# Kernel tuning notes

Measured on AMD Instinct MI355X. Metric: run time of the kernel, lower is better.

Reference implementation:

```python
import jax, jax.numpy as jnp
import numpy as np

B, S, DM, H, DF = 2, 2048, 1024, 16, 4096
HD = DM // H
EPS = 1e-6
NEG = -1e9


def setup_inputs() -> dict:
    key = jax.random.key(0)
    ks = jax.random.split(key, 16)
    sc = 1.0 / np.sqrt(DM)
    scf = 1.0 / np.sqrt(DF)
    return {
        "x": jax.random.normal(ks[0], (B, S, DM), jnp.float32),
        "src_mask": jax.random.randint(ks[1], (B, 1, 1, S), 0, 2, jnp.int32),
        "Wq": jax.random.normal(ks[2], (DM, DM), jnp.float32) * sc,
        "bq": jnp.zeros((DM,), jnp.float32),
        "Wk": jax.random.normal(ks[3], (DM, DM), jnp.float32) * sc,
        "bk": jnp.zeros((DM,), jnp.float32),
        "Wv": jax.random.normal(ks[4], (DM, DM), jnp.float32) * sc,
        "bv": jnp.zeros((DM,), jnp.float32),
        "Wo": jax.random.normal(ks[5], (DM, DM), jnp.float32) * sc,
        "bo": jnp.zeros((DM,), jnp.float32),
        "W1": jax.random.normal(ks[6], (DM, DF), jnp.float32) * sc,
        "b1": jnp.zeros((DF,), jnp.float32),
        "W2": jax.random.normal(ks[7], (DF, DM), jnp.float32) * scf,
        "b2": jnp.zeros((DM,), jnp.float32),
        "alpha1": jnp.ones((1,), jnp.float32),
        "beta1": jnp.ones((1,), jnp.float32),
        "alpha2": jnp.ones((1,), jnp.float32),
        "beta2": jnp.ones((1,), jnp.float32),
    }


def layer_norm(x, alpha, beta):
    # torch: mean + unbiased std (ddof=1), scalar alpha/beta, eps added to std
    mean = jnp.mean(x, axis=-1, keepdims=True)
    std = jnp.std(x, axis=-1, keepdims=True, ddof=1)
    return alpha * (x - mean) / (std + EPS) + beta


def mha(x, mask, Wq, bq, Wk, bk, Wv, bv, Wo, bo):
    def split(t):  # [B,S,DM] -> [B,H,S,HD]
        return t.reshape(B, S, H, HD).transpose(0, 2, 1, 3)
    q = split(x @ Wq + bq)
    k = split(x @ Wk + bk)
    v = split(x @ Wv + bv)
    scores = jnp.einsum("bhqd,bhkd->bhqk", q, k) / np.sqrt(HD)
    scores = jnp.where(mask == 0, NEG, scores)
    probs = jax.nn.softmax(scores, axis=-1)  # dropout in eval mode = identity
    out = jnp.einsum("bhqk,bhkd->bhqd", probs, v)
    out = out.transpose(0, 2, 1, 3).reshape(B, S, DM)
    return out @ Wo + bo


def reference(x, src_mask, Wq, bq, Wk, bk, Wv, bv, Wo, bo, W1, b1, W2, b2,
              alpha1, beta1, alpha2, beta2):
    # pre-norm residual: x + attn(norm(x)); dropout disabled (eval)
    n1 = layer_norm(x, alpha1, beta1)
    h = x + mha(n1, src_mask, Wq, bq, Wk, bk, Wv, bv, Wo, bo)
    n2 = layer_norm(h, alpha2, beta2)
    ff = jax.nn.relu(n2 @ W1 + b1) @ W2 + b2
    return h + ff
```

## Files before the change

### kernel.cpp

```cpp
#include <hip/hip_runtime.h>
#include <hip/hip_bf16.h>

#define SEQ   2048
#define BATCH 2
#define DMODEL 1024
#define DFF   4096
#define NHEAD 16
#define HDIM  64
#define NTOK  (BATCH*SEQ)

typedef short s8v __attribute__((ext_vector_type(8)));
typedef float f4v __attribute__((ext_vector_type(4)));

__device__ __forceinline__ float b2f(unsigned short u) {
    union { unsigned int i; float f; } v; v.i = ((unsigned int)u) << 16; return v.f;
}
__device__ __forceinline__ unsigned short f2b(float f) {
    union { unsigned int i; float f; } v; v.f = f;
    unsigned int r = v.i + 0x7FFFu + ((v.i >> 16) & 1u);
    return (unsigned short)(r >> 16);
}
__device__ __forceinline__ ushort2 cvt_pk(float a, float b) {
    __hip_bfloat162 h = __float22bfloat162_rn(float2{ a, b });
    return *(ushort2*)&h;
}

__device__ __forceinline__ f4v mfma_bf16(s8v a, s8v b, f4v c) {
    return __builtin_amdgcn_mfma_f32_16x16x32_bf16(a, b, c, 0, 0, 0);
}

__device__ __forceinline__ void gload_lds16(const void* g, void* l) {
    __builtin_amdgcn_global_load_lds(
        (const __attribute__((address_space(1))) unsigned int*)g,
        (__attribute__((address_space(3))) unsigned int*)l, 16, 0, 0);
}

template<int N> __device__ __forceinline__ void wait_vmcnt() {
    if constexpr (N == 8)      asm volatile("s_waitcnt vmcnt(8)" ::: "memory");
    else if constexpr (N == 6) asm volatile("s_waitcnt vmcnt(6)" ::: "memory");
    else if constexpr (N == 4) asm volatile("s_waitcnt vmcnt(4)" ::: "memory");
    else if constexpr (N == 2) asm volatile("s_waitcnt vmcnt(2)" ::: "memory");
    else                       asm volatile("s_waitcnt vmcnt(0)" ::: "memory");
}

__device__ __forceinline__ void tp_tile(const float* __restrict__ src,
                                        unsigned short* __restrict__ dst,
                                        int R, int C, int br, int bc, int t,
                                        unsigned short* tl) {
    for (int i = 0; i < 4; i++) {
        int lin = i * 1024 + t * 4;
        int r = lin >> 6, c = lin & 63;
        float4 u = *(const float4*)&src[(size_t)(br * 64 + r) * C + bc * 64 + c];
        tl[r * 65 + c + 0] = f2b(u.x);
        tl[r * 65 + c + 1] = f2b(u.y);
        tl[r * 65 + c + 2] = f2b(u.z);
        tl[r * 65 + c + 3] = f2b(u.w);
    }
    __syncthreads();
    for (int i = 0; i < 4; i++) {
        int lin = i * 1024 + t * 4;
        int r2 = lin >> 6, c2 = lin & 63;
        ushort4 o;
        o.x = tl[(c2 + 0) * 65 + r2];
        o.y = tl[(c2 + 1) * 65 + r2];
        o.z = tl[(c2 + 2) * 65 + r2];
        o.w = tl[(c2 + 3) * 65 + r2];
        *(ushort4*)&dst[(size_t)(bc * 64 + r2) * R + br * 64 + c2] = o;
    }
}

__global__ __launch_bounds__(256) void prep_weights(const float* __restrict__ Wq,
                                                    const float* __restrict__ Wk,
                                                    const float* __restrict__ Wv,
                                                    const float* __restrict__ Wo,
                                                    const float* __restrict__ W1,
                                                    const float* __restrict__ W2,
                                                    const float* __restrict__ bq,
                                                    const float* __restrict__ bk,
                                                    const float* __restrict__ bv,
                                                    const float* __restrict__ x,
                                                    const float* __restrict__ a1,
                                                    const float* __restrict__ be1,
                                                    unsigned short* __restrict__ Wqkv_t,
                                                    unsigned short* __restrict__ Wo_t,
                                                    unsigned short* __restrict__ W1_t,
                                                    unsigned short* __restrict__ W2_t,
                                                    float* __restrict__ bqkv,
                                                    unsigned short* __restrict__ n1) {
    __shared__ unsigned short tl[64 * 65];
    __shared__ float red[8];
    const int t = threadIdx.x;
    const int bx = blockIdx.x, by = blockIdx.y, z = blockIdx.z;
    if (z < 4) {
        const float* src = (z == 0) ? Wq : (z == 1) ? Wk : (z == 2) ? Wv : Wo;
        unsigned short* dst = (z == 3) ? Wo_t : Wqkv_t + (size_t)z * 1024 * 1024;
        tp_tile(src, dst, 1024, 1024, bx, by, t, tl);
    } else if (z == 4) {
        for (int i = 0; i < 4; i++) {
            tp_tile(W1, W1_t, 1024, 4096, bx, by + 16 * i, t, tl);
            __syncthreads();
        }
    } else if (z == 5) {
        if (bx == 0 && by == 0) {
            for (int i = 0; i < 12; i++) {
                int idx = t + 256 * i;
                if (idx < 1024) bqkv[idx] = bq[idx];
                else if (idx < 2048) bqkv[idx] = bk[idx - 1024];
                else if (idx < 3072) bqkv[idx] = bv[idx - 2048];
            }
        }
        for (int i = 0; i < 4; i++) {
            tp_tile(W2, W2_t, 4096, 1024, bx + 16 * i, by, t, tl);
            __syncthreads();
        }
    } else {
        const int row = (z - 6) * 256 + by * 16 + bx;
        const float* xr = x + (size_t)row * DMODEL;
        float4 u = ((const float4*)xr)[t];
        float v[4] = { u.x, u.y, u.z, u.w };
        float s = v[0] + v[1] + v[2] + v[3];
        float sq = v[0]*v[0] + v[1]*v[1] + v[2]*v[2] + v[3]*v[3];
        for (int off = 32; off; off >>= 1) { s += __shfl_xor(s, off); sq += __shfl_xor(sq, off); }
        int wave = t >> 6, lane = t & 63;
        if (!lane) { red[wave] = s; red[4 + wave] = sq; }
        __syncthreads();
        s = red[0] + red[1] + red[2] + red[3];
        sq = red[4] + red[5] + red[6] + red[7];
        float mean = s * (1.f / DMODEL);
        float var = (sq - (float)DMODEL * mean * mean) * (1.f / (DMODEL - 1));
        var = var < 0.f ? 0.f : var;
        float inv = a1[0] / (sqrtf(var) + 1e-6f);
        float bt = be1[0];
        uint2 ou;
        unsigned short r0 = f2b((v[0] - mean) * inv + bt);
        unsigned short r1 = f2b((v[1] - mean) * inv + bt);
        unsigned short r2 = f2b((v[2] - mean) * inv + bt);
        unsigned short r3 = f2b((v[3] - mean) * inv + bt);
        ou.x = (unsigned int)r0 | ((unsigned int)r1 << 16);
        ou.y = (unsigned int)r2 | ((unsigned int)r3 << 16);
        ((uint2*)(n1 + (size_t)row * DMODEL))[t] = ou;
    }
}

__global__ __launch_bounds__(256) void mask_scan(const int* __restrict__ msk,
                                                 int* __restrict__ idx,
                                                 float* __restrict__ maskc2,
                                                 int* __restrict__ ntiles) {
    const int b = blockIdx.x, t = threadIdx.x;
    const int base = b * SEQ;
    __shared__ int wsum[4];
    int k[8]; int cnt = 0;
    for (int j = 0; j < 8; j++) {
        k[j] = (msk[base + t * 8 + j] != 0) ? 1 : 0;
        cnt += k[j];
    }
    const int lane = t & 63, wv = t >> 6;
    int pre = cnt;
    for (int off = 1; off < 64; off <<= 1) {
        int n = __shfl_up(pre, off);
        if (lane >= off) pre += n;
    }
    if (lane == 63) wsum[wv] = pre;
    __syncthreads();
    const int Nb = wsum[0] + wsum[1] + wsum[2] + wsum[3];
    int woff = 0;
    for (int w = 0; w < wv; w++) woff += wsum[w];
    const int excl = woff + pre - cnt;
    for (int j = 0; j < 8; j++) {
        int g = t * 8 + j;
        idx[base + g] = 0;
        maskc2[base + g] = (g < Nb) ? 0.f : -1e9f;
    }
    __syncthreads();
    int pos = excl;
    for (int j = 0; j < 8; j++) {
        if (k[j]) { idx[base + pos] = t * 8 + j; pos++; }
    }
    if (t == 0) ntiles[b] = (Nb + 63) >> 6;
}

__global__ __launch_bounds__(256) void pack_kv(const unsigned short* __restrict__ Kb,
                                               const unsigned short* __restrict__ Vb,
                                               const int* __restrict__ idx,
                                               const int* __restrict__ ntiles,
                                               unsigned short* __restrict__ Kc,
                                               unsigned short* __restrict__ Vc) {
    __shared__ unsigned short tl[64 * 65];
    const int t = threadIdx.x;
    const int kt = blockIdx.x, h = blockIdx.y, b = blockIdx.z;
    if (kt >= ntiles[b]) return;
    const int* idxb = idx + b * SEQ + kt * 64;
    const unsigned short* srcK = Kb + (size_t)b * SEQ * 1024 + h * HDIM;
    unsigned short* dstK = Kc + ((size_t)((b * NHEAD + h) * 32 + kt)) * 4096;
    for (int i = 0; i < 2; i++) {
        int ci = t + 256 * i;
        int r = ci >> 3, cp = ci & 7;
        int cl = cp ^ (r & 7);
        int row = idxb[r];
        *(uint4*)&dstK[ci * 8] = *(const uint4*)&srcK[(size_t)row * 1024 + cl * 8];
    }
    const unsigned short* srcV = Vb + (size_t)b * SEQ * 1024 + h * HDIM;
    for (int i = 0; i < 16; i++) {
        int idx2 = t + 256 * i;
        int r = idx2 >> 6, c = idx2 & 63;
        int row = idxb[r];
        tl[r * 65 + c] = srcV[(size_t)row * 1024 + c];
    }
    __syncthreads();
    unsigned short* dstV = Vc + ((size_t)((b * NHEAD + h) * 32 + kt)) * 4096;
    for (int i = 0; i < 2; i++) {
        int ci = t + 256 * i;
        int r = ci >> 3, cp = ci & 7;
        int cl = cp ^ (r & 7);
        ushort4 e0, e1;
        e0.x = tl[(cl * 8 + 0) * 65 + r]; e0.y = tl[(cl * 8 + 1) * 65 + r];
        e0.z = tl[(cl * 8 + 2) * 65 + r]; e0.w = tl[(cl * 8 + 3) * 65 + r];
        e1.x = tl[(cl * 8 + 4) * 65 + r]; e1.y = tl[(cl * 8 + 5) * 65 + r];
        e1.z = tl[(cl * 8 + 6) * 65 + r]; e1.w = tl[(cl * 8 + 7) * 65 + r];
        *(ushort4*)&dstV[ci * 8]     = e0;
        *(ushort4*)&dstV[ci * 8 + 4] = e1;
    }
}

__global__ __launch_bounds__(256) void ln_add(float* __restrict__ hb,
                                              const float* __restrict__ pbuf,
                                              const float* __restrict__ al,
                                              const float* __restrict__ be,
                                              unsigned short* __restrict__ o) {
    const int row = blockIdx.x;
    float* hr = hb + (size_t)row * DMODEL;
    const float* pr = pbuf + (size_t)row * DMODEL;
    float4 u = ((const float4*)hr)[threadIdx.x];
    float4 p = ((const float4*)pr)[threadIdx.x];
    u.x += p.x; u.y += p.y; u.z += p.z; u.w += p.w;
    ((float4*)hr)[threadIdx.x] = u;
    float v[4] = { u.x, u.y, u.z, u.w };
    float s = v[0] + v[1] + v[2] + v[3];
    float sq = v[0]*v[0] + v[1]*v[1] + v[2]*v[2] + v[3]*v[3];
    for (int off = 32; off; off >>= 1) { s += __shfl_xor(s, off); sq += __shfl_xor(sq, off); }
    __shared__ float red[8];
    int wave = threadIdx.x >> 6, lane = threadIdx.x & 63;
    if (!lane) { red[wave] = s; red[4 + wave] = sq; }
    __syncthreads();
    s = red[0] + red[1] + red[2] + red[3];
    sq = red[4] + red[5] + red[6] + red[7];
    float mean = s * (1.f / DMODEL);
    float var = (sq - (float)DMODEL * mean * mean) * (1.f / (DMODEL - 1));
    var = var < 0.f ? 0.f : var;
    float inv = al[0] / (sqrtf(var) + 1e-6f);
    float bt = be[0];
    uint2 ou;
    unsigned short r0 = f2b((v[0] - mean) * inv + bt);
    unsigned short r1 = f2b((v[1] - mean) * inv + bt);
    unsigned short r2 = f2b((v[2] - mean) * inv + bt);
    unsigned short r3 = f2b((v[3] - mean) * inv + bt);
    ou.x = (unsigned int)r0 | ((unsigned int)r1 << 16);
    ou.y = (unsigned int)r2 | ((unsigned int)r3 << 16);
    ((uint2*)(o + (size_t)row * DMODEL))[threadIdx.x] = ou;
}

__global__ __launch_bounds__(256) void add_pbuf(float* __restrict__ out,
                                                const float* __restrict__ pbuf) {
    const int i0 = (blockIdx.x * 256 + threadIdx.x) * 8;
    float4 a0 = *(const float4*)&out[i0];
    float4 a1 = *(const float4*)&out[i0 + 4];
    float4 p0 = *(const float4*)&pbuf[i0];
    float4 p1 = *(const float4*)&pbuf[i0 + 4];
    a0.x += p0.x; a0.y += p0.y; a0.z += p0.z; a0.w += p0.w;
    a1.x += p1.x; a1.y += p1.y; a1.z += p1.z; a1.w += p1.w;
    *(float4*)&out[i0]     = a0;
    *(float4*)&out[i0 + 4] = a1;
}

template<int SPAN, int NL>
__device__ __forceinline__ void stage_half(const unsigned short* __restrict__ mat,
                                           int base, int K, int k0, int q,
                                           unsigned short* sdst, int t) {
#pragma unroll
    for (int i = 0; i < NL; i++) {
        int ci = i * 512 + t;
        int rl = ci >> 3;
        int c  = (ci & 7) ^ (rl & 7);
        int gr = (rl / SPAN) * (2 * SPAN) + q * SPAN + (rl % SPAN);
        gload_lds16(mat + (size_t)(base + gr) * K + k0 + c * 8, sdst + (size_t)ci * 8);
    }
}

__device__ __forceinline__ const s8v* afrag(const unsigned short* sA, int mi, int s,
                                            int wm, int l16, int quad) {
    int q = mi >> 2;
    int rl = wm * 64 + (mi & 3) * 16 + l16;
    return (const s8v*)&sA[q * 8192 + rl * 64 + (((s * 4 + quad) ^ (l16 & 7)) * 8)];
}
__device__ __forceinline__ const s8v* bfrag(const unsigned short* sB, int ni, int s,
                                            int wn, int l16, int quad) {
    int q = ni >> 1;
    int rl = wn * 32 + (ni & 1) * 16 + l16;
    return (const s8v*)&sB[q * 8192 + rl * 64 + (((s * 4 + quad) ^ (l16 & 7)) * 8)];
}

__device__ __forceinline__ void half_8ph(const unsigned short* __restrict__ A,
                                         const unsigned short* __restrict__ Bt,
                                         int m0, int n0, int K, int kT1, int kT2, bool doT2,
                                         const unsigned short* sAr, const unsigned short* sBr,
                                         unsigned short* sA_this, unsigned short* sB_this,
                                         unsigned short* sA_oth,
                                         int wm, int wn, int l16, int quad, int t,
                                         f4v acc[8][4]) {
    s8v a[4][2], b[4][2];
#pragma unroll
    for (int m2 = 0; m2 < 4; m2++) {
        a[m2][0] = *afrag(sAr, m2, 0, wm, l16, quad);
        a[m2][1] = *afrag(sAr, m2, 1, wm, l16, quad);
    }
#pragma unroll
    for (int nb = 0; nb < 2; nb++) {
        b[nb][0] = *bfrag(sBr, nb, 0, wn, l16, quad);
        b[nb][1] = *bfrag(sBr, nb, 1, wn, l16, quad);
    }
    stage_half<64, 2>(A, m0, K, kT1, 1, sA_oth + 8192, t);
    __builtin_amdgcn_s_barrier();
    asm volatile("s_waitcnt lgkmcnt(0)" ::: "memory");
    __builtin_amdgcn_s_setprio(1);
#pragma unroll
    for (int m2 = 0; m2 < 4; m2++)
#pragma unroll
        for (int nb = 0; nb < 2; nb++) {
            acc[m2][nb] = mfma_bf16(a[m2][0], b[nb][0], acc[m2][nb]);
            acc[m2][nb] = mfma_bf16(a[m2][1], b[nb][1], acc[m2][nb]);
        }
    __builtin_amdgcn_s_setprio(0);
    __builtin_amdgcn_s_barrier();
#pragma unroll
    for (int nb = 0; nb < 2; nb++) {
        b[2 + nb][0] = *bfrag(sBr, 2 + nb, 0, wn, l16, quad);
        b[2 + nb][1] = *bfrag(sBr, 2 + nb, 1, wn, l16, quad);
    }
    if (doT2) stage_half<64, 2>(A, m0, K, kT2, 0, sA_this, t);
    __builtin_amdgcn_s_barrier();
    asm volatile("s_waitcnt lgkmcnt(0)" ::: "memory");
    __builtin_amdgcn_s_setprio(1);
#pragma unroll
    for (int m2 = 0; m2 < 4; m2++)
#pragma unroll
        for (int nb = 0; nb < 2; nb++) {
            acc[m2][2 + nb] = mfma_bf16(a[m2][0], b[2 + nb][0], acc[m2][2 + nb]);
            acc[m2][2 + nb] = mfma_bf16(a[m2][1], b[2 + nb][1], acc[m2][2 + nb]);
        }
    __builtin_amdgcn_s_setprio(0);
    __builtin_amdgcn_s_barrier();
#pragma unroll
    for (int m2 = 0; m2 < 4; m2++) {
        a[m2][0] = *afrag(sAr, 4 + m2, 0, wm, l16, quad);
        a[m2][1] = *afrag(sAr, 4 + m2, 1, wm, l16, quad);
    }
    if (doT2) stage_half<32, 2>(Bt, n0, K, kT2, 0, sB_this, t);
    __builtin_amdgcn_s_barrier();
    asm volatile("s_waitcnt lgkmcnt(0)" ::: "memory");
    __builtin_amdgcn_s_setprio(1);
#pragma unroll
    for (int m2 = 0; m2 < 4; m2++)
#pragma unroll
        for (int nb = 0; nb < 2; nb++) {
            acc[4 + m2][nb] = mfma_bf16(a[m2][0], b[nb][0], acc[4 + m2][nb]);
            acc[4 + m2][nb] = mfma_bf16(a[m2][1], b[nb][1], acc[4 + m2][nb]);
        }
    __builtin_amdgcn_s_setprio(0);
    __builtin_amdgcn_s_barrier();
    if (doT2) {
        stage_half<32, 2>(Bt, n0, K, kT2, 1, sB_this + 8192, t);
        wait_vmcnt<6>();
    } else {
        wait_vmcnt<0>();
    }
    __builtin_amdgcn_s_barrier();
    __builtin_amdgcn_s_setprio(1);
#pragma unroll
    for (int m2 = 0; m2 < 4; m2++)
#pragma unroll
        for (int nb = 0; nb < 2; nb++) {
            acc[4 + m2][2 + nb] = mfma_bf16(a[m2][0], b[2 + nb][0], acc[4 + m2][2 + nb]);
            acc[4 + m2][2 + nb] = mfma_bf16(a[m2][1], b[2 + nb][1], acc[4 + m2][2 + nb]);
        }
    __builtin_amdgcn_s_setprio(0);
    __builtin_amdgcn_s_barrier();
}

__device__ __forceinline__ void comp_full(const unsigned short* sA, const unsigned short* sB,
                                          int wm, int wn, int l16, int quad,
                                          f4v acc[8][4]) {
    s8v b[4][2];
#pragma unroll
    for (int ni = 0; ni < 4; ni++) {
        b[ni][0] = *bfrag(sB, ni, 0, wn, l16, quad);
        b[ni][1] = *bfrag(sB, ni, 1, wn, l16, quad);
    }
#pragma unroll
    for (int mi = 0; mi < 8; mi++) {
        s8v a0 = *afrag(sA, mi, 0, wm, l16, quad);
        s8v a1 = *afrag(sA, mi, 1, wm, l16, quad);
#pragma unroll
        for (int ni = 0; ni < 4; ni++) {
            acc[mi][ni] = mfma_bf16(a0, b[ni][0], acc[mi][ni]);
            acc[mi][ni] = mfma_bf16(a1, b[ni][1], acc[mi][ni]);
        }
    }
}

template<bool RELU, typename CT, bool SPLIT3>
__global__ __launch_bounds__(512, 2) void gemm256(const unsigned short* __restrict__ A,
                                                  const unsigned short* __restrict__ Bt,
                                                  const float* __restrict__ bias,
                                                  CT* __restrict__ C,
                                                  int M, int N, int K) {
    __shared__ __align__(16) unsigned short smA[2][256 * 64];
    __shared__ __align__(16) unsigned short smB[2][256 * 64];
    const int t = threadIdx.x;
    const int wave = t >> 6, lane = t & 63;
    const int quad = lane >> 4, l16 = lane & 15;
    const int wm = wave >> 2, wn = wave & 3;
    const int m0 = blockIdx.x * 256, n0 = blockIdx.y * 256;
    const int nt = K >> 6;

    f4v acc[8][4] = {};

    stage_half<64, 2>(A, m0, K, 0, 0, smA[0], t);
    stage_half<64, 2>(A, m0, K, 0, 1, smA[0] + 8192, t);
    stage_half<32, 2>(Bt, n0, K, 0, 0, smB[0], t);
    stage_half<32, 2>(Bt, n0, K, 0, 1, smB[0] + 8192, t);
    stage_half<64, 2>(A, m0, K, 64, 0, smA[1], t);
    stage_half<32, 2>(Bt, n0, K, 64, 0, smB[1], t);
    stage_half<32, 2>(Bt, n0, K, 64, 1, smB[1] + 8192, t);
    wait_vmcnt<6>();
    __builtin_amdgcn_s_barrier();

    for (int i = 0; i < nt / 2 - 1; ++i) {
        const int kb = 2 * i * 64;
        half_8ph(A, Bt, m0, n0, K, kb + 64, kb + 128, true,
                 smA[0], smB[0], smA[0], smB[0], smA[1],
                 wm, wn, l16, quad, t, acc);
        half_8ph(A, Bt, m0, n0, K, kb + 128, kb + 192, true,
                 smA[1], smB[1], smA[1], smB[1], smA[0],
                 wm, wn, l16, quad, t, acc);
    }
    half_8ph(A, Bt, m0, n0, K, (nt - 1) * 64, 0, false,
             smA[0], smB[0], smA[0], smB[0], smA[1],
             wm, wn, l16, quad, t, acc);
    __builtin_amdgcn_s_setprio(1);
    comp_full(smA[1], smB[1], wm, wn, l16, quad, acc);
    __builtin_amdgcn_s_setprio(0);

#pragma unroll
    for (int mi = 0; mi < 8; mi++) {
#pragma unroll
        for (int ni = 0; ni < 4; ni++) {
            const int col = n0 + wn * 64 + ni * 16 + l16;
            const int row0 = m0 + wm * 128 + mi * 16 + quad * 4;
            const float bv = bias[col];
#pragma unroll
            for (int r = 0; r < 4; r++) {
                float v = acc[mi][ni][r] + bv;
                if (RELU) v = v > 0.f ? v : 0.f;
                size_t cidx;
                if constexpr (SPLIT3)
                    cidx = (size_t)(col >> 10) * ((size_t)NTOK * 1024)
                         + (size_t)row0 * 1024 + (size_t)r * 1024 + (col & 1023);
                else
                    cidx = (size_t)(row0 + r) * N + col;
                if constexpr (sizeof(CT) == 2)
                    C[cidx] = f2b(v);
                else
                    C[cidx] = v;
            }
        }
    }
}


__device__ __forceinline__ void stage128(const unsigned short* __restrict__ mat,
                                         int base, int K, int k0,
                                         unsigned short* sdst, int t) {
#pragma unroll
    for (int q = 0; q < 2; q++) {
        int rl = t >> 3;
        int c  = (t & 7) ^ (rl & 7);
        gload_lds16(mat + (size_t)(base + q * 64 + rl) * K + k0 + c * 8,
                    sdst + q * 4096 + (size_t)t * 8);
    }
}

__device__ __forceinline__ s8v rdfrag128(const unsigned short* sm, int q, int fi,
                                         int l16, int quad, int sW) {
    int rl = fi * 16 + l16;
    int p = (sW * 4 + quad) ^ (l16 & 7);
    return *(const s8v*)&sm[q * 4096 + rl * 64 + p * 8];
}

__global__ __launch_bounds__(512, 4) void gemm128k(const unsigned short* __restrict__ A,
                                                   const unsigned short* __restrict__ Bt,
                                                   const float* __restrict__ bias,
                                                   const float* __restrict__ res,
                                                   float* __restrict__ C,
                                                   float* __restrict__ pbuf,
                                                   int M, int N, int K, int KS) {
    __shared__ __align__(16) unsigned short smem[4][8192];
    const int t = threadIdx.x;
    const int wave = t >> 6, lane = t & 63;
    const int quad = lane >> 4, l16 = lane & 15;
    const int sW = wave >> 2, wm = (wave >> 1) & 1, wn = wave & 1;
    const int m0 = blockIdx.x * 128, n0 = blockIdx.y * 128;
    const int z = blockIdx.z;
    const int kbeg = z * KS;
    const int nt = KS >> 6;

    f4v acc[4][4] = {};

    stage128(A,  m0, K, kbeg,      smem[0], t);
    stage128(Bt, n0, K, kbeg,      smem[2], t);
    stage128(A,  m0, K, kbeg + 64, smem[1], t);
    stage128(Bt, n0, K, kbeg + 64, smem[3], t);
    wait_vmcnt<4>();
    __builtin_amdgcn_s_barrier();

    for (int it = 0; it < nt; ++it) {
        const int cb = it & 1;
        const unsigned short* sA = smem[cb];
        const unsigned short* sB = smem[2 + cb];
        s8v a[4], b[4];
#pragma unroll
        for (int i = 0; i < 4; i++) a[i] = rdfrag128(sA, wm, i, l16, quad, sW);
#pragma unroll
        for (int i = 0; i < 4; i++) b[i] = rdfrag128(sB, wn, i, l16, quad, sW);
        asm volatile("s_waitcnt lgkmcnt(0)" ::: "memory");
        __builtin_amdgcn_s_setprio(1);
#pragma unroll
        for (int mi = 0; mi < 4; mi++)
#pragma unroll
            for (int ni = 0; ni < 4; ni++)
                acc[mi][ni] = mfma_bf16(a[mi], b[ni], acc[mi][ni]);
        __builtin_amdgcn_s_setprio(0);
        __builtin_amdgcn_s_barrier();
        if (it + 2 < nt) {
            stage128(A,  m0, K, kbeg + (it + 2) * 64, smem[cb], t);
            stage128(Bt, n0, K, kbeg + (it + 2) * 64, smem[2 + cb], t);
            wait_vmcnt<4>();
        } else if (it + 1 < nt) {
            wait_vmcnt<0>();
        }
        __builtin_amdgcn_s_barrier();
    }

    float* xch = (float*)&smem[0][0];
    float* myx = xch + (wm * 2 + wn) * 4096;
    if (sW == 1) {
#pragma unroll
        for (int mi = 0; mi < 4; mi++)
#pragma unroll
            for (int ni = 0; ni < 4; ni++)
                *(f4v*)&myx[(mi * 4 + ni) * 256 + lane * 4] = acc[mi][ni];
    }
    __builtin_amdgcn_s_barrier();
    if (sW == 0) {
#pragma unroll
        for (int mi = 0; mi < 4; mi++)
#pragma unroll
            for (int ni = 0; ni < 4; ni++)
                acc[mi][ni] += *(const f4v*)&myx[(mi * 4 + ni) * 256 + lane * 4];
#pragma unroll
        for (int mi = 0; mi < 4; mi++)
#pragma unroll
            for (int ni = 0; ni < 4; ni++) {
                const int col = n0 + wn * 64 + ni * 16 + l16;
                const int row0 = m0 + wm * 64 + mi * 16 + quad * 4;
                if (z == 0) {
                    const float bv = bias[col];
#pragma unroll
                    for (int r = 0; r < 4; r++) {
                        size_t ix = (size_t)(row0 + r) * N + col;
                        C[ix] = acc[mi][ni][r] + bv + res[ix];
                    }
                } else {
#pragma unroll
                    for (int r = 0; r < 4; r++)
                        pbuf[(size_t)(row0 + r) * N + col] = acc[mi][ni][r];
                }
            }
    }
}

#define EXPC 0.18033688f
__device__ __forceinline__ void attn_tile(const unsigned short* __restrict__ smKb,
                                          const unsigned short* __restrict__ smVb,
                                          const float* __restrict__ smM, int k0,
                                          unsigned short* __restrict__ smPw,
                                          s8v qf0, s8v qf1, int quad, int l16,
                                          float& l_s, f4v* oacc) {
    const int l7 = l16 & 7;
    f4v s[4];
#pragma unroll
    for (int kt4 = 0; kt4 < 4; kt4++) {
        int r = kt4 * 16 + l16;
        s8v kf0 = *(const s8v*)&smKb[r * 64 + ((quad ^ l7) * 8)];
        s8v kf1 = *(const s8v*)&smKb[r * 64 + (((quad + 4) ^ l7) * 8)];
        f4v z = {};
        z = mfma_bf16(kf0, qf0, z);
        z = mfma_bf16(kf1, qf1, z);
        s[kt4] = z;
    }
#pragma unroll
    for (int kt4 = 0; kt4 < 4; kt4++) {
        float4 mf = *(const float4*)&smM[k0 + kt4 * 16 + quad * 4];
        s[kt4][0] = s[kt4][0] * EXPC + mf.x;
        s[kt4][1] = s[kt4][1] * EXPC + mf.y;
        s[kt4][2] = s[kt4][2] * EXPC + mf.z;
        s[kt4][3] = s[kt4][3] * EXPC + mf.w;
    }
#pragma unroll
    for (int kt4 = 0; kt4 < 4; kt4++)
#pragma unroll
        for (int r = 0; r < 4; r++) {
            float p = __builtin_amdgcn_exp2f(s[kt4][r]);
            s[kt4][r] = p;
            l_s += p;
        }
#pragma unroll
    for (int kt4 = 0; kt4 < 4; kt4++) {
        ushort2 p01 = cvt_pk(s[kt4][0], s[kt4][1]);
        ushort2 p23 = cvt_pk(s[kt4][2], s[kt4][3]);
        ushort4 pk;
        pk.x = p01.x; pk.y = p01.y; pk.z = p23.x; pk.w = p23.y;
        int c = kt4 * 2 + (quad >> 1);
        *(ushort4*)&smPw[l16 * 64 + ((c ^ l7) * 8 + (quad & 1) * 4)] = pk;
    }
    s8v pf0 = *(const s8v*)&smPw[l16 * 64 + ((quad ^ l7) * 8)];
    s8v pf1 = *(const s8v*)&smPw[l16 * 64 + (((quad + 4) ^ l7) * 8)];
#pragma unroll
    for (int nt = 0; nt < 4; nt++) {
        int r = nt * 16 + l16;
        s8v v0 = *(const s8v*)&smVb[r * 64 + ((quad ^ l7) * 8)];
        s8v v1 = *(const s8v*)&smVb[r * 64 + (((quad + 4) ^ l7) * 8)];
        oacc[nt] = mfma_bf16(pf0, v0, oacc[nt]);
        oacc[nt] = mfma_bf16(pf1, v1, oacc[nt]);
    }
}

__global__ __launch_bounds__(512) void attn_kernel(const unsigned short* __restrict__ Qb,
                                                   const unsigned short* __restrict__ Kc,
                                                   const unsigned short* __restrict__ Vc,
                                                   const float* __restrict__ maskc2,
                                                   const int* __restrict__ ntiles,
                                                   unsigned short* __restrict__ out) {
    __shared__ __align__(16) unsigned short smK[2][4096];
    __shared__ __align__(16) unsigned short smV[2][4096];
    __shared__ __align__(16) unsigned short smP[8][1024];
    __shared__ __align__(16) float smM[SEQ];

    const int t = threadIdx.x;
    const int wave = t >> 6, lane = t & 63;
    const int quad = lane >> 4, l16 = lane & 15;
    const int qt = blockIdx.x, h = blockIdx.y, b = blockIdx.z;
    const int q0 = qt * 128 + wave * 16;
    const int nt = ntiles[b];
    const unsigned short* Kbh = Kc + ((size_t)(b * NHEAD + h)) * 32 * 4096;
    const unsigned short* Vbh = Vc + ((size_t)(b * NHEAD + h)) * 32 * 4096;
    unsigned short* smPw = &smP[wave][0];

    const unsigned short* Qp = Qb + ((size_t)b * SEQ + q0 + l16) * 1024 + h * HDIM + quad * 8;
    s8v qf0 = *(const s8v*)(Qp);
    s8v qf1 = *(const s8v*)(Qp + 32);

    gload_lds16(maskc2 + (size_t)b * SEQ + t * 4, (float*)smM + t * 4);
    gload_lds16(Kbh + t * 8,        smK[0] + t * 8);
    gload_lds16(Vbh + t * 8,        smV[0] + t * 8);
    gload_lds16(Kbh + 4096 + t * 8, smK[1] + t * 8);
    gload_lds16(Vbh + 4096 + t * 8, smV[1] + t * 8);
    wait_vmcnt<2>();
    __builtin_amdgcn_s_barrier();

    float l_s = 0.f;
    f4v oacc[4] = {};

    for (int it = 0; it < nt; ++it) {
        const int cb = it & 1;
        __builtin_amdgcn_s_setprio(1);
        attn_tile(smK[cb], smV[cb], smM, it * 64, smPw, qf0, qf1, quad, l16, l_s, oacc);
        __builtin_amdgcn_s_setprio(0);
        if (it + 2 < nt) {
            asm volatile("s_waitcnt lgkmcnt(0)" ::: "memory");
            __builtin_amdgcn_s_barrier();
            gload_lds16(Kbh + (size_t)(it + 2) * 4096 + t * 8, smK[cb] + t * 8);
            gload_lds16(Vbh + (size_t)(it + 2) * 4096 + t * 8, smV[cb] + t * 8);
            wait_vmcnt<2>();
            __builtin_amdgcn_s_barrier();
        } else if (it + 1 < nt) {
            asm volatile("s_waitcnt lgkmcnt(0)" ::: "memory");
            __builtin_amdgcn_s_barrier();
            wait_vmcnt<0>();
            __builtin_amdgcn_s_barrier();
        }
    }

    l_s += __shfl_xor(l_s, 16);
    l_s += __shfl_xor(l_s, 32);
    float lrr[4];
    for (int r = 0; r < 4; r++) lrr[r] = __shfl(l_s, quad * 4 + r);
    for (int nt2 = 0; nt2 < 4; nt2++)
        for (int r = 0; r < 4; r++) {
            int row = q0 + quad * 4 + r;
            int col = h * HDIM + nt2 * 16 + l16;
            out[((size_t)b * SEQ + row) * DMODEL + col] = f2b(oacc[nt2][r] / lrr[r]);
        }
}

extern "C" void kernel_launch(void* const* d_in, const int* in_sizes, int n_in,
                              void* d_out, int out_size, void* d_ws, size_t ws_size,
                              hipStream_t stream) {
    const float* x   = (const float*)d_in[0];
    const int*   msk = (const int*)d_in[1];
    const float* Wq  = (const float*)d_in[2];
    const float* bq  = (const float*)d_in[3];
    const float* Wk  = (const float*)d_in[4];
    const float* bk  = (const float*)d_in[5];
    const float* Wv  = (const float*)d_in[6];
    const float* bv  = (const float*)d_in[7];
    const float* Wo  = (const float*)d_in[8];
    const float* bo  = (const float*)d_in[9];
    const float* W1  = (const float*)d_in[10];
    const float* b1  = (const float*)d_in[11];
    const float* W2  = (const float*)d_in[12];
    const float* b2  = (const float*)d_in[13];
    const float* a1  = (const float*)d_in[14];
    const float* be1 = (const float*)d_in[15];
    const float* a2  = (const float*)d_in[16];
    const float* be2 = (const float*)d_in[17];
    float* outf = (float*)d_out;

    char* ws = (char*)d_ws;
    const size_t MB = 1024 * 1024;
    unsigned short* W2_t   = (unsigned short*)(ws);
    unsigned short* W1_t   = (unsigned short*)(ws + 8 * MB);
    float*          Pbuf   = (float*)(ws + 8 * MB);
    unsigned short* Wqkv_t = (unsigned short*)(ws + 16 * MB);
    float*          bqkv   = (float*)(ws + 22 * MB);
    unsigned short* Kc     = (unsigned short*)(ws + 16 * MB);
    unsigned short* n2     = (unsigned short*)(ws + 16 * MB);
    unsigned short* Wo_t   = (unsigned short*)(ws + 24 * MB);
    unsigned short* Qb     = (unsigned short*)(ws + 26 * MB);
    unsigned short* Kb     = (unsigned short*)(ws + 34 * MB);
    unsigned short* Vb     = (unsigned short*)(ws + 42 * MB);
    float*          Pbuf2  = (float*)(ws + 34 * MB);
    unsigned short* ff1    = (unsigned short*)(ws + 26 * MB);
    unsigned short* attnO  = (unsigned short*)(ws + 50 * MB);
    unsigned short* n1     = (unsigned short*)d_out;
    unsigned short* Vc     = (unsigned short*)d_out;
    float*          hbuf   = (float*)d_out;
    float*          maskc2 = (float*)((char*)d_out + 8 * MB);
    int*            idxc   = (int*)((char*)d_out + 8 * MB + 16 * 1024);
    int*            ntl    = (int*)((char*)d_out + 8 * MB + 32 * 1024);

    mask_scan<<<dim3(BATCH), 256, 0, stream>>>(msk, idxc, maskc2, ntl);
    prep_weights<<<dim3(16, 16, 22), 256, 0, stream>>>(
        Wq, Wk, Wv, Wo, W1, W2, bq, bk, bv, x, a1, be1,
        Wqkv_t, Wo_t, W1_t, W2_t, bqkv, n1);

    gemm256<false, unsigned short, true><<<dim3(16, 12), 512, 0, stream>>>(
        n1, Wqkv_t, bqkv, Qb, NTOK, 3072, 1024);
    pack_kv<<<dim3(32, 16, 2), 256, 0, stream>>>(Kb, Vb, idxc, ntl, Kc, Vc);
    attn_kernel<<<dim3(16, 16, 2), 512, 0, stream>>>(Qb, Kc, Vc, maskc2, ntl, attnO);
    gemm128k<<<dim3(32, 8, 2), 512, 0, stream>>>(
        attnO, Wo_t, bo, x, hbuf, Pbuf2, NTOK, 1024, 1024, 512);
    ln_add<<<NTOK, 256, 0, stream>>>(hbuf, Pbuf2, a2, be2, n2);
    gemm256<true, unsigned short, false><<<dim3(16, 16), 512, 0, stream>>>(
        n2, W1_t, b1, ff1, NTOK, DFF, 1024);
    gemm128k<<<dim3(32, 8, 2), 512, 0, stream>>>(
        ff1, W2_t, b2, hbuf, outf, Pbuf, NTOK, 1024, 4096, 2048);
    add_pbuf<<<dim3(2048), 256, 0, stream>>>(outf, Pbuf);
}
```

Before: 327.5 us.

## Fold mask scan into prep kernel, swizzle block order, move LDS wait after MFMAs

```diff
diff --git a/kernel.cpp b/kernel.cpp
--- a/kernel.cpp
+++ b/kernel.cpp
@@ -81,14 +81,19 @@
                                                     const float* __restrict__ x,
                                                     const float* __restrict__ a1,
                                                     const float* __restrict__ be1,
+                                                    const int* __restrict__ msk,
                                                     unsigned short* __restrict__ Wqkv_t,
                                                     unsigned short* __restrict__ Wo_t,
                                                     unsigned short* __restrict__ W1_t,
                                                     unsigned short* __restrict__ W2_t,
                                                     float* __restrict__ bqkv,
-                                                    unsigned short* __restrict__ n1) {
+                                                    unsigned short* __restrict__ n1,
+                                                    int* __restrict__ idxc,
+                                                    float* __restrict__ maskc2,
+                                                    int* __restrict__ ntl) {
     __shared__ unsigned short tl[64 * 65];
     __shared__ float red[8];
+    __shared__ int wsum[4];
     const int t = threadIdx.x;
     const int bx = blockIdx.x, by = blockIdx.y, z = blockIdx.z;
     if (z < 4) {
@@ -113,6 +118,38 @@
             tp_tile(W2, W2_t, 4096, 1024, bx + 16 * i, by, t, tl);
             __syncthreads();
         }
+    } else if (z == 22) {
+        if (bx >= BATCH || by != 0) return;
+        const int b = bx;
+        const int base = b * SEQ;
+        int k[8]; int cnt = 0;
+        for (int j = 0; j < 8; j++) {
+            k[j] = (msk[base + t * 8 + j] != 0) ? 1 : 0;
+            cnt += k[j];
+        }
+        const int lane = t & 63, wv = t >> 6;
+        int pre = cnt;
+        for (int off = 1; off < 64; off <<= 1) {
+            int n = __shfl_up(pre, off);
+            if (lane >= off) pre += n;
+        }
+        if (lane == 63) wsum[wv] = pre;
+        __syncthreads();
+        const int Nb = wsum[0] + wsum[1] + wsum[2] + wsum[3];
+        int woff = 0;
+        for (int w = 0; w < wv; w++) woff += wsum[w];
+        const int excl = woff + pre - cnt;
+        for (int j = 0; j < 8; j++) {
+            int g = t * 8 + j;
+            idxc[base + g] = 0;
+            maskc2[base + g] = (g < Nb) ? 0.f : -1e9f;
+        }
+        __syncthreads();
+        int pos = excl;
+        for (int j = 0; j < 8; j++) {
+            if (k[j]) { idxc[base + pos] = t * 8 + j; pos++; }
+        }
+        if (t == 0) ntl[b] = (Nb + 63) >> 6;
     } else {
         const int row = (z - 6) * 256 + by * 16 + bx;
         const float* xr = x + (size_t)row * DMODEL;
@@ -140,43 +177,6 @@
         ou.y = (unsigned int)r2 | ((unsigned int)r3 << 16);
         ((uint2*)(n1 + (size_t)row * DMODEL))[t] = ou;
     }
-}
-
-__global__ __launch_bounds__(256) void mask_scan(const int* __restrict__ msk,
-                                                 int* __restrict__ idx,
-                                                 float* __restrict__ maskc2,
-                                                 int* __restrict__ ntiles) {
-    const int b = blockIdx.x, t = threadIdx.x;
-    const int base = b * SEQ;
-    __shared__ int wsum[4];
-    int k[8]; int cnt = 0;
-    for (int j = 0; j < 8; j++) {
-        k[j] = (msk[base + t * 8 + j] != 0) ? 1 : 0;
-        cnt += k[j];
-    }
-    const int lane = t & 63, wv = t >> 6;
-    int pre = cnt;
-    for (int off = 1; off < 64; off <<= 1) {
-        int n = __shfl_up(pre, off);
-        if (lane >= off) pre += n;
-    }
-    if (lane == 63) wsum[wv] = pre;
-    __syncthreads();
-    const int Nb = wsum[0] + wsum[1] + wsum[2] + wsum[3];
-    int woff = 0;
-    for (int w = 0; w < wv; w++) woff += wsum[w];
-    const int excl = woff + pre - cnt;
-    for (int j = 0; j < 8; j++) {
-        int g = t * 8 + j;
-        idx[base + g] = 0;
-        maskc2[base + g] = (g < Nb) ? 0.f : -1e9f;
-    }
-    __syncthreads();
-    int pos = excl;
-    for (int j = 0; j < 8; j++) {
-        if (k[j]) { idx[base + pos] = t * 8 + j; pos++; }
-    }
-    if (t == 0) ntiles[b] = (Nb + 63) >> 6;
 }
 
 __global__ __launch_bounds__(256) void pack_kv(const unsigned short* __restrict__ Kb,
@@ -464,7 +464,7 @@
                 size_t cidx;
                 if constexpr (SPLIT3)
                     cidx = (size_t)(col >> 10) * ((size_t)NTOK * 1024)
-                         + (size_t)row0 * 1024 + (size_t)r * 1024 + (col & 1023);
+                         + (size_t)(row0 + r) * 1024 + (col & 1023);
                 else
                     cidx = (size_t)(row0 + r) * N + col;
                 if constexpr (sizeof(CT) == 2)
@@ -508,8 +508,11 @@
     const int wave = t >> 6, lane = t & 63;
     const int quad = lane >> 4, l16 = lane & 15;
     const int sW = wave >> 2, wm = (wave >> 1) & 1, wn = wave & 1;
-    const int m0 = blockIdx.x * 128, n0 = blockIdx.y * 128;
-    const int z = blockIdx.z;
+    const int lin = blockIdx.x + (blockIdx.y << 6);
+    const int swz = (lin & 7) * 64 + (lin >> 3);
+    const int z  = swz & 1;
+    const int m0 = ((swz >> 1) & 31) * 128;
+    const int n0 = (swz >> 6) * 128;
     const int kbeg = z * KS;
     const int nt = KS >> 6;
 
@@ -531,7 +534,6 @@
         for (int i = 0; i < 4; i++) a[i] = rdfrag128(sA, wm, i, l16, quad, sW);
 #pragma unroll
         for (int i = 0; i < 4; i++) b[i] = rdfrag128(sB, wn, i, l16, quad, sW);
-        asm volatile("s_waitcnt lgkmcnt(0)" ::: "memory");
         __builtin_amdgcn_s_setprio(1);
 #pragma unroll
         for (int mi = 0; mi < 4; mi++)
@@ -539,6 +541,7 @@
             for (int ni = 0; ni < 4; ni++)
                 acc[mi][ni] = mfma_bf16(a[mi], b[ni], acc[mi][ni]);
         __builtin_amdgcn_s_setprio(0);
+        asm volatile("s_waitcnt lgkmcnt(0)" ::: "memory");
         __builtin_amdgcn_s_barrier();
         if (it + 2 < nt) {
             stage128(A,  m0, K, kbeg + (it + 2) * 64, smem[cb], t);
@@ -658,7 +661,9 @@
     const int t = threadIdx.x;
     const int wave = t >> 6, lane = t & 63;
     const int quad = lane >> 4, l16 = lane & 15;
-    const int qt = blockIdx.x, h = blockIdx.y, b = blockIdx.z;
+    const int lin = blockIdx.x + (blockIdx.y << 4) + (blockIdx.z << 8);
+    const int swz = (lin & 7) * 64 + (lin >> 3);
+    const int qt = swz & 15, h = (swz >> 4) & 15, b = swz >> 8;
     const int q0 = qt * 128 + wave * 16;
     const int nt = ntiles[b];
     const unsigned short* Kbh = Kc + ((size_t)(b * NHEAD + h)) * 32 * 4096;
@@ -758,21 +763,20 @@
     int*            idxc   = (int*)((char*)d_out + 8 * MB + 16 * 1024);
     int*            ntl    = (int*)((char*)d_out + 8 * MB + 32 * 1024);
 
-    mask_scan<<<dim3(BATCH), 256, 0, stream>>>(msk, idxc, maskc2, ntl);
-    prep_weights<<<dim3(16, 16, 22), 256, 0, stream>>>(
-        Wq, Wk, Wv, Wo, W1, W2, bq, bk, bv, x, a1, be1,
-        Wqkv_t, Wo_t, W1_t, W2_t, bqkv, n1);
+    prep_weights<<<dim3(16, 16, 23), 256, 0, stream>>>(
+        Wq, Wk, Wv, Wo, W1, W2, bq, bk, bv, x, a1, be1, msk,
+        Wqkv_t, Wo_t, W1_t, W2_t, bqkv, n1, idxc, maskc2, ntl);
 
     gemm256<false, unsigned short, true><<<dim3(16, 12), 512, 0, stream>>>(
         n1, Wqkv_t, bqkv, Qb, NTOK, 3072, 1024);
     pack_kv<<<dim3(32, 16, 2), 256, 0, stream>>>(Kb, Vb, idxc, ntl, Kc, Vc);
     attn_kernel<<<dim3(16, 16, 2), 512, 0, stream>>>(Qb, Kc, Vc, maskc2, ntl, attnO);
-    gemm128k<<<dim3(32, 8, 2), 512, 0, stream>>>(
+    gemm128k<<<dim3(64, 8), 512, 0, stream>>>(
         attnO, Wo_t, bo, x, hbuf, Pbuf2, NTOK, 1024, 1024, 512);
     ln_add<<<NTOK, 256, 0, stream>>>(hbuf, Pbuf2, a2, be2, n2);
     gemm256<true, unsigned short, false><<<dim3(16, 16), 512, 0, stream>>>(
         n2, W1_t, b1, ff1, NTOK, DFF, 1024);
-    gemm128k<<<dim3(32, 8, 2), 512, 0, stream>>>(
+    gemm128k<<<dim3(64, 8), 512, 0, stream>>>(
         ff1, W2_t, b2, hbuf, outf, Pbuf, NTOK, 1024, 4096, 2048);
     add_pbuf<<<dim3(2048), 256, 0, stream>>>(outf, Pbuf);
 }
```

Result: no change. 333.0 us (+1.7%).
